# Kernel tuning notes

Measured on AMD Instinct MI355X. Metric: run time of the kernel, lower is better.

Reference implementation:

```python
import jax, jax.numpy as jnp
import numpy as np

D_MODEL = 1024


def setup_inputs() -> dict:
    key = jax.random.key(0)
    ks = jax.random.split(key, 7)
    x = jax.random.normal(ks[0], (4, 2048, D_MODEL), dtype=jnp.float32)
    scale = 1.0 / np.sqrt(D_MODEL)
    Wq = jax.random.normal(ks[1], (D_MODEL, D_MODEL), dtype=jnp.float32) * scale
    bq = jnp.zeros((D_MODEL,), dtype=jnp.float32)
    Wk = jax.random.normal(ks[2], (D_MODEL, D_MODEL), dtype=jnp.float32) * scale
    bk = jnp.zeros((D_MODEL,), dtype=jnp.float32)
    Wv = jax.random.normal(ks[3], (D_MODEL, D_MODEL), dtype=jnp.float32) * scale
    bv = jnp.zeros((D_MODEL,), dtype=jnp.float32)
    return {"x": x, "Wq": Wq, "bq": bq, "Wk": Wk, "bk": bk, "Wv": Wv, "bv": bv}


def reference(x, Wq, bq, Wk, bk, Wv, bv):
    # Linear layers: y = x @ W^T + b (torch nn.Linear convention)
    q = jnp.einsum("bsd,ed->bse", x, Wq) + bq
    k = jnp.einsum("bsd,ed->bse", x, Wk) + bk
    v = jnp.einsum("bsd,ed->bse", x, Wv) + bv
    d_k = q.shape[-1]
    inv_sqrt_dk = 1.0 / jnp.sqrt(jnp.float32(d_k))
    # [B, S, S] score matrix, softmax over keys, then AV
    score = jnp.einsum("bqd,bkd->bqk", q, k) * inv_sqrt_dk
    attn = jax.nn.softmax(score, axis=-1)
    out = jnp.einsum("bqk,bkd->bqd", attn, v)
    return out
```

## Files before the change

kernel.cpp:

```cpp
#include <hip/hip_runtime.h>
#include <hip/hip_bf16.h>


typedef __hip_bfloat16 bf16;
typedef __attribute__((ext_vector_type(8))) short bf16x8;
typedef __attribute__((ext_vector_type(4))) float f32x4;
typedef __attribute__((ext_vector_type(4))) short short4v;

__device__ __forceinline__ void gload16(const bf16* g, bf16* l) {
  __builtin_amdgcn_global_load_lds(
      (const __attribute__((address_space(1))) void*)g,
      (__attribute__((address_space(3))) void*)l, 16, 0, 0);
}

__global__ __launch_bounds__(256)
void cast_f32_to_bf16(const float* __restrict__ in, bf16* __restrict__ out) {
  long i = ((long)blockIdx.x * blockDim.x + threadIdx.x) * 4;
  float4 f = *(const float4*)(in + i);
  bf16 tmp[4];
  tmp[0] = __float2bfloat16(f.x);
  tmp[1] = __float2bfloat16(f.y);
  tmp[2] = __float2bfloat16(f.z);
  tmp[3] = __float2bfloat16(f.w);
  *(short4v*)(out + i) = *(short4v*)tmp;
}

__global__ __launch_bounds__(256)
void cast3_f32_to_bf16(const float* __restrict__ w0, const float* __restrict__ w1,
                       const float* __restrict__ w2, bf16* __restrict__ out) {
  const float* src = (blockIdx.y == 0) ? w0 : (blockIdx.y == 1) ? w1 : w2;
  long i = ((long)blockIdx.x * blockDim.x + threadIdx.x) * 4;
  float4 f = *(const float4*)(src + i);
  bf16 tmp[4];
  tmp[0] = __float2bfloat16(f.x);
  tmp[1] = __float2bfloat16(f.y);
  tmp[2] = __float2bfloat16(f.z);
  tmp[3] = __float2bfloat16(f.w);
  *(short4v*)(out + (long)blockIdx.y * 1024 * 1024 + i) = *(short4v*)tmp;
}

template<int OMODE>
__global__ __launch_bounds__(256, 3)
void gemm_bt(const bf16* __restrict__ A, const bf16* __restrict__ Bt,
             const float* __restrict__ b0, const float* __restrict__ b1,
             const float* __restrict__ b2, void* __restrict__ Cout,
             int K, int lda, int ldb, int ldc, float scale,
             long sA, long sB, long sC)
{
  __shared__ __align__(16) bf16 As[128 * 64];
  __shared__ __align__(16) bf16 Bs[128 * 64];
  const int tid = threadIdx.x;
  const int z = blockIdx.z;
  const bf16* Ab = A + (long)z * sA;
  const bf16* Bb = Bt + (long)z * sB;
  const long bm = (long)blockIdx.x * 128;
  const long bn = (long)blockIdx.y * 128;
  const int wid = tid >> 6;
  const int lane = tid & 63;
  const int wr = (wid >> 1) * 64;
  const int wc = (wid & 1) * 64;
  const int l15 = lane & 15;
  const int kg = lane >> 4;

  f32x4 acc[4][4];
#pragma unroll
  for (int m = 0; m < 4; ++m)
#pragma unroll
    for (int n = 0; n < 4; ++n)
      acc[m][n] = (f32x4){0.f, 0.f, 0.f, 0.f};

  for (int k0 = 0; k0 < K; k0 += 64) {
#pragma unroll
    for (int i = 0; i < 4; ++i) {
      const int c = (i << 8) + tid;
      const int r = c >> 3;
      const int j = (c & 7) ^ (r & 7);
      const int ldsch = (i << 8) + (wid << 6);
      gload16(Ab + (long)(bm + r) * lda + k0 + (j << 3), As + ldsch * 8);
      gload16(Bb + (long)(bn + r) * ldb + k0 + (j << 3), Bs + ldsch * 8);
    }
    __syncthreads();
#pragma unroll
    for (int kk = 0; kk < 2; ++kk) {
      bf16x8 af[4], bfv[4];
#pragma unroll
      for (int m = 0; m < 4; ++m) {
        const int row_l = wr + (m << 4) + l15;
        const int js = ((kk << 2) + kg) ^ (row_l & 7);
        af[m] = *(const bf16x8*)&As[(row_l << 6) + (js << 3)];
      }
#pragma unroll
      for (int n = 0; n < 4; ++n) {
        const int row_l = wc + (n << 4) + l15;
        const int js = ((kk << 2) + kg) ^ (row_l & 7);
        bfv[n] = *(const bf16x8*)&Bs[(row_l << 6) + (js << 3)];
      }
#pragma unroll
      for (int m = 0; m < 4; ++m)
#pragma unroll
        for (int n = 0; n < 4; ++n)
          acc[m][n] = __builtin_amdgcn_mfma_f32_16x16x32_bf16(
              af[m], bfv[n], acc[m][n], 0, 0, 0);
    }
    __syncthreads();
  }

#pragma unroll
  for (int m = 0; m < 4; ++m) {
    const long row0 = bm + wr + (m << 4) + (kg << 2);
#pragma unroll
    for (int n = 0; n < 4; ++n) {
      const long col = bn + wc + (n << 4) + l15;
      const float* bias = (z == 0) ? b0 : (z == 1) ? b1 : b2;
      const float bias_v = bias[col];
      if (z < 2) {
        bf16* C = (bf16*)Cout + (long)z * 8192 * 1024;
#pragma unroll
        for (int rr = 0; rr < 4; ++rr)
          C[(row0 + rr) * 1024 + col] =
              __float2bfloat16(acc[m][n][rr] + bias_v);
      } else {
        bf16* C = (bf16*)Cout + 2L * 8192 * 1024;
        const long bb = row0 >> 11;
        const long s0 = row0 & 2047;
        bf16 tmp[4];
#pragma unroll
        for (int rr = 0; rr < 4; ++rr)
          tmp[rr] = __float2bfloat16(acc[m][n][rr] + bias_v);
        *(short4v*)&C[(bb * 1024 + col) * 2048 + s0] = *(short4v*)tmp;
      }
    }
  }
}

template<int OMODE>
__global__ __launch_bounds__(512, 4)
void gemm8w(const bf16* __restrict__ A, const bf16* __restrict__ Bt,
            void* __restrict__ Cout, int K, int lda, int ldb, int ldc,
            float scale, long sA, long sB, long sC)
{
  __shared__ __align__(16) bf16 As[128 * 64 + 6144];
  __shared__ __align__(16) bf16 Bs[128 * 64 + 6144];
  const int tid = threadIdx.x;
  const int z = blockIdx.z;
  const bf16* Ab = A + (long)z * sA;
  const bf16* Bb = Bt + (long)z * sB;
  const long bm = (long)blockIdx.x * 128;
  const long bn = (long)blockIdx.y * 128;
  const int wid = tid >> 6;
  const int lane = tid & 63;
  const int wr = (wid >> 2) * 64;
  const int wc = (wid & 3) * 32;
  const int l15 = lane & 15;
  const int kg = lane >> 4;

  f32x4 acc[4][2];
#pragma unroll
  for (int m = 0; m < 4; ++m)
#pragma unroll
    for (int n = 0; n < 2; ++n)
      acc[m][n] = (f32x4){0.f, 0.f, 0.f, 0.f};

  for (int k0 = 0; k0 < K; k0 += 64) {
#pragma unroll
    for (int i = 0; i < 2; ++i) {
      const int c = (i << 9) + tid;
      const int r = c >> 3;
      const int j = (c & 7) ^ (r & 7);
      const int ldsch = (i << 9) + (wid << 6);
      gload16(Ab + (long)(bm + r) * lda + k0 + (j << 3), As + ldsch * 8);
      gload16(Bb + (long)(bn + r) * ldb + k0 + (j << 3), Bs + ldsch * 8);
    }
    __syncthreads();
#pragma unroll
    for (int kk = 0; kk < 2; ++kk) {
      bf16x8 af[4], bfv[2];
#pragma unroll
      for (int m = 0; m < 4; ++m) {
        const int row_l = wr + (m << 4) + l15;
        const int js = ((kk << 2) + kg) ^ (row_l & 7);
        af[m] = *(const bf16x8*)&As[(row_l << 6) + (js << 3)];
      }
#pragma unroll
      for (int n = 0; n < 2; ++n) {
        const int row_l = wc + (n << 4) + l15;
        const int js = ((kk << 2) + kg) ^ (row_l & 7);
        bfv[n] = *(const bf16x8*)&Bs[(row_l << 6) + (js << 3)];
      }
#pragma unroll
      for (int m = 0; m < 4; ++m)
#pragma unroll
        for (int n = 0; n < 2; ++n)
          acc[m][n] = __builtin_amdgcn_mfma_f32_16x16x32_bf16(
              af[m], bfv[n], acc[m][n], 0, 0, 0);
    }
    __syncthreads();
  }

#pragma unroll
  for (int m = 0; m < 4; ++m) {
    const long row0 = bm + wr + (m << 4) + (kg << 2);
#pragma unroll
    for (int n = 0; n < 2; ++n) {
      const long col = bn + wc + (n << 4) + l15;
      if constexpr (OMODE == 0) {
        float* C = (float*)Cout + (long)z * sC;
#pragma unroll
        for (int rr = 0; rr < 4; ++rr)
          C[(row0 + rr) * ldc + col] = acc[m][n][rr] * scale;
      } else {
        bf16* C = (bf16*)Cout + (long)z * sC;
#pragma unroll
        for (int rr = 0; rr < 4; ++rr)
          C[(row0 + rr) * ldc + col] = __float2bfloat16(acc[m][n][rr] * scale);
      }
    }
  }
}

__global__ __launch_bounds__(256)
void softmax_bf16(bf16* __restrict__ S) {
  bf16* row = S + (size_t)blockIdx.x * 2048;
  const int tid = threadIdx.x;
  __shared__ float redA[4], redB[4];
  bf16x8 in = *(const bf16x8*)(row + (tid << 3));
  float v[8];
  float mx = -1e30f;
#pragma unroll
  for (int i = 0; i < 8; ++i) {
    v[i] = __bfloat162float(((const bf16*)&in)[i]);
    mx = fmaxf(mx, v[i]);
  }
#pragma unroll
  for (int o = 32; o; o >>= 1) mx = fmaxf(mx, __shfl_xor(mx, o));
  if ((tid & 63) == 0) redA[tid >> 6] = mx;
  __syncthreads();
  mx = fmaxf(fmaxf(redA[0], redA[1]), fmaxf(redA[2], redA[3]));
  float sum = 0.f;
#pragma unroll
  for (int i = 0; i < 8; ++i) {
    v[i] = __expf(v[i] - mx);
    sum += v[i];
  }
#pragma unroll
  for (int o = 32; o; o >>= 1) sum += __shfl_xor(sum, o);
  if ((tid & 63) == 0) redB[tid >> 6] = sum;
  __syncthreads();
  sum = redB[0] + redB[1] + redB[2] + redB[3];
  const float inv = 1.f / sum;
  bf16 tmp[8];
#pragma unroll
  for (int i = 0; i < 8; ++i) tmp[i] = __float2bfloat16(v[i] * inv);
  *(bf16x8*)(row + (tid << 3)) = *(bf16x8*)tmp;
}

extern "C" void kernel_launch(void* const* d_in, const int* in_sizes, int n_in,
                              void* d_out, int out_size, void* d_ws, size_t ws_size,
                              hipStream_t stream) {
  const float* x  = (const float*)d_in[0];
  const float* Wq = (const float*)d_in[1];
  const float* bq = (const float*)d_in[2];
  const float* Wk = (const float*)d_in[3];
  const float* bk = (const float*)d_in[4];
  const float* Wv = (const float*)d_in[5];
  const float* bv = (const float*)d_in[6];
  float* out = (float*)d_out;

  const int B = 4, S = 2048, D = 1024;
  const int M = B * S;

  bf16* xb  = (bf16*)d_ws;
  bf16* wqb = xb + (size_t)M * D;
  bf16* qb  = wqb + 3 * (size_t)D * D;
  bf16* kb  = qb + (size_t)M * D;
  bf16* vtb = kb + (size_t)M * D;
  bf16* sc  = vtb + (size_t)M * D;

  size_t avail = ws_size - ((size_t)((char*)sc - (char*)d_ws));
  int nb = (int)(avail / ((size_t)S * S * 2));
  if (nb > B) nb = B;
  if (nb < 1) nb = 1;

  cast_f32_to_bf16<<<dim3(M * D / 1024), 256, 0, stream>>>(x, xb);
  cast3_f32_to_bf16<<<dim3(D * D / 1024, 3), 256, 0, stream>>>(Wq, Wk, Wv, wqb);

  gemm_bt<3><<<dim3(M / 128, D / 128, 3), 256, 0, stream>>>(
      xb, wqb, bq, bk, bv, qb, D, D, D, D, 1.f, 0, (long)D * D, 0);

  const float iscale = 1.0f / 32.0f;
  for (int g = 0; g < B; g += nb) {
    const int gn = (g + nb <= B) ? nb : (B - g);
    gemm8w<1><<<dim3(S / 128, S / 128, gn), 512, 0, stream>>>(
        qb + (size_t)g * S * D, kb + (size_t)g * S * D,
        sc, D, D, D, S, iscale, (long)S * D, (long)S * D, (long)S * S);
    softmax_bf16<<<dim3(gn * S), 256, 0, stream>>>(sc);
    gemm8w<0><<<dim3(S / 128, D / 128, gn), 512, 0, stream>>>(
        sc, vtb + (size_t)g * D * S,
        out + (size_t)g * S * D, S, S, S, D, 1.f,
        (long)S * S, (long)D * S, (long)S * D);
  }
}
```

Baseline: 172.3 us.

## Add 256x256 double-buffered phased GEMM kernel for QK^T score computation

Adds a new 8-wave kernel that computes the Q·K^T scores with 256x256 output tiles. It double-buffers LDS through direct global-to-LDS loads and splits each K step into four MFMA quadrants, interleaved with prefetches, explicit waitcnt, barriers and setprio. The aim is to hide global load latency behind MFMA work and to raise data reuse per tile. In exchange it uses 128KB of LDS and many accumulator registers, which limits occupancy to one block per CU, and it launches only 64 blocks per batch. The QKV and AV kernels get cleanup only: templates are removed and parameters simplified.

```diff
diff --git a/kernel.cpp b/kernel.cpp
--- a/kernel.cpp
+++ b/kernel.cpp
@@ -12,6 +12,13 @@
       (const __attribute__((address_space(1))) void*)g,
       (__attribute__((address_space(3))) void*)l, 16, 0, 0);
 }
+
+#define WAITV(N) asm volatile("s_waitcnt vmcnt(" #N ")" ::: "memory")
+#define LGKM0    asm volatile("s_waitcnt lgkmcnt(0)" ::: "memory")
+#define SCHED0   __builtin_amdgcn_sched_barrier(0)
+#define BAR      __builtin_amdgcn_s_barrier()
+#define PRIO1    __builtin_amdgcn_s_setprio(1)
+#define PRIO0    __builtin_amdgcn_s_setprio(0)
 
 __global__ __launch_bounds__(256)
 void cast_f32_to_bf16(const float* __restrict__ in, bf16* __restrict__ out) {
@@ -39,35 +46,29 @@
   *(short4v*)(out + (long)blockIdx.y * 1024 * 1024 + i) = *(short4v*)tmp;
 }
 
-template<int OMODE>
 __global__ __launch_bounds__(256, 3)
-void gemm_bt(const bf16* __restrict__ A, const bf16* __restrict__ Bt,
-             const float* __restrict__ b0, const float* __restrict__ b1,
-             const float* __restrict__ b2, void* __restrict__ Cout,
-             int K, int lda, int ldb, int ldc, float scale,
-             long sA, long sB, long sC)
+void gemm_qkv(const bf16* __restrict__ A, const bf16* __restrict__ Bt,
+              const float* __restrict__ b0, const float* __restrict__ b1,
+              const float* __restrict__ b2, void* __restrict__ Cout,
+              int K, int lda, int ldb, long sB)
 {
   __shared__ __align__(16) bf16 As[128 * 64];
   __shared__ __align__(16) bf16 Bs[128 * 64];
   const int tid = threadIdx.x;
   const int z = blockIdx.z;
-  const bf16* Ab = A + (long)z * sA;
+  const bf16* Ab = A;
   const bf16* Bb = Bt + (long)z * sB;
   const long bm = (long)blockIdx.x * 128;
   const long bn = (long)blockIdx.y * 128;
-  const int wid = tid >> 6;
-  const int lane = tid & 63;
-  const int wr = (wid >> 1) * 64;
-  const int wc = (wid & 1) * 64;
-  const int l15 = lane & 15;
-  const int kg = lane >> 4;
+  const int wid = tid >> 6, lane = tid & 63;
+  const int wr = (wid >> 1) * 64, wc = (wid & 1) * 64;
+  const int l15 = lane & 15, kg = lane >> 4;
 
   f32x4 acc[4][4];
 #pragma unroll
   for (int m = 0; m < 4; ++m)
 #pragma unroll
-    for (int n = 0; n < 4; ++n)
-      acc[m][n] = (f32x4){0.f, 0.f, 0.f, 0.f};
+    for (int n = 0; n < 4; ++n) acc[m][n] = (f32x4){0.f, 0.f, 0.f, 0.f};
 
   for (int k0 = 0; k0 < K; k0 += 64) {
 #pragma unroll
@@ -117,8 +118,7 @@
         bf16* C = (bf16*)Cout + (long)z * 8192 * 1024;
 #pragma unroll
         for (int rr = 0; rr < 4; ++rr)
-          C[(row0 + rr) * 1024 + col] =
-              __float2bfloat16(acc[m][n][rr] + bias_v);
+          C[(row0 + rr) * 1024 + col] = __float2bfloat16(acc[m][n][rr] + bias_v);
       } else {
         bf16* C = (bf16*)Cout + 2L * 8192 * 1024;
         const long bb = row0 >> 11;
@@ -134,6 +134,130 @@
 }
 
 template<int OMODE>
+__global__ __launch_bounds__(512)
+void gemm8ph(const bf16* __restrict__ A, const bf16* __restrict__ Bt,
+             void* __restrict__ Cout, int K, int lda, int ldb, int ldc,
+             float scale, long sA, long sB, long sC)
+{
+  __shared__ __align__(16) bf16 As[2][2][128 * 64];
+  __shared__ __align__(16) bf16 Bs[2][2][128 * 64];
+  const int tid = threadIdx.x;
+  const int wid = tid >> 6, lane = tid & 63;
+  const int l15 = lane & 15, kg = lane >> 4;
+  const int wr = wid >> 2;
+  const int wc = wid & 3;
+  const int bh = wc >> 1;
+  const int z = blockIdx.z;
+  const bf16* Ab = A + (long)z * sA;
+  const bf16* Bb = Bt + (long)z * sB;
+  const long bm = (long)blockIdx.x * 256;
+  const long bn = (long)blockIdx.y * 256;
+
+  const bf16* gAp[2][2];
+  const bf16* gBp[2][2];
+  int dOff[2];
+#pragma unroll
+  for (int l = 0; l < 2; ++l) {
+    const int c = (l << 9) + tid;
+    const int r = c >> 3;
+    const int j = (c & 7) ^ (r & 7);
+#pragma unroll
+    for (int h = 0; h < 2; ++h) {
+      gAp[h][l] = Ab + (long)(bm + h * 128 + r) * lda + (j << 3);
+      gBp[h][l] = Bb + (long)(bn + h * 128 + r) * ldb + (j << 3);
+    }
+    dOff[l] = (((l << 9) + (wid << 6)) << 3);
+  }
+#define STG_A(H, BUF, TT) do { const int _k = (TT) << 6;            \
+    gload16(gAp[H][0] + _k, &As[BUF][H][dOff[0]]);                  \
+    gload16(gAp[H][1] + _k, &As[BUF][H][dOff[1]]); } while (0)
+#define STG_B(H, BUF, TT) do { const int _k = (TT) << 6;            \
+    gload16(gBp[H][0] + _k, &Bs[BUF][H][dOff[0]]);                  \
+    gload16(gBp[H][1] + _k, &Bs[BUF][H][dOff[1]]); } while (0)
+
+  bf16x8 af[2][4], bv[2][2][2];
+  f32x4 acc[8][4];
+#pragma unroll
+  for (int m = 0; m < 8; ++m)
+#pragma unroll
+    for (int n = 0; n < 4; ++n) acc[m][n] = (f32x4){0.f, 0.f, 0.f, 0.f};
+
+#define READA(MH, BUF) do { _Pragma("unroll") for (int kk = 0; kk < 2; ++kk) \
+    _Pragma("unroll") for (int mi = 0; mi < 4; ++mi) {                       \
+      const int row = (MH) * 64 + mi * 16 + l15;                             \
+      const int js = ((kk << 2) + kg) ^ (row & 7);                           \
+      af[kk][mi] = *(const bf16x8*)&As[BUF][wr][(row << 6) + (js << 3)];     \
+    } } while (0)
+#define READB(NH, BUF) do { _Pragma("unroll") for (int kk = 0; kk < 2; ++kk) \
+    _Pragma("unroll") for (int ni = 0; ni < 2; ++ni) {                       \
+      const int row = (wc & 1) * 64 + ((NH) * 2 + ni) * 16 + l15;            \
+      const int js = ((kk << 2) + kg) ^ (row & 7);                           \
+      bv[NH][kk][ni] = *(const bf16x8*)&Bs[BUF][bh][(row << 6) + (js << 3)]; \
+    } } while (0)
+#define MFMAQ(MH, NH) do { _Pragma("unroll") for (int kk = 0; kk < 2; ++kk)  \
+    _Pragma("unroll") for (int mi = 0; mi < 4; ++mi)                         \
+    _Pragma("unroll") for (int ni = 0; ni < 2; ++ni)                         \
+      acc[(MH)*4+mi][(NH)*2+ni] = __builtin_amdgcn_mfma_f32_16x16x32_bf16(   \
+          af[kk][mi], bv[NH][kk][ni], acc[(MH)*4+mi][(NH)*2+ni], 0, 0, 0);   \
+  } while (0)
+
+  const int T = K >> 6;
+  STG_B(0, 0, 0); STG_B(1, 0, 0); STG_A(0, 0, 0); STG_A(1, 0, 0);
+  STG_B(0, 1, 1); STG_B(1, 1, 1);
+  WAITV(4); BAR;
+
+  for (int t = 0; t < T; t += 2) {
+    const bool pre = (t + 2) < T;
+    READA(0, 0); READB(0, 0);
+    STG_A(0, 1, t + 1);
+    BAR; LGKM0; SCHED0; PRIO1; MFMAQ(0, 0); PRIO0; BAR;
+    READB(1, 0);
+    STG_A(1, 1, t + 1);
+    BAR; LGKM0; SCHED0; PRIO1; MFMAQ(0, 1); PRIO0; BAR;
+    READA(1, 0);
+    if (pre) STG_B(0, 0, t + 2);
+    BAR; LGKM0; SCHED0; PRIO1; MFMAQ(1, 0); PRIO0; BAR;
+    if (pre) { STG_B(1, 0, t + 2); WAITV(4); } else { WAITV(0); }
+    BAR; PRIO1; MFMAQ(1, 1); PRIO0; BAR;
+    READA(0, 1); READB(0, 1);
+    if (pre) STG_A(0, 0, t + 2);
+    BAR; LGKM0; SCHED0; PRIO1; MFMAQ(0, 0); PRIO0; BAR;
+    READB(1, 1);
+    if (pre) STG_A(1, 0, t + 2);
+    BAR; LGKM0; SCHED0; PRIO1; MFMAQ(0, 1); PRIO0; BAR;
+    READA(1, 1);
+    if (pre) STG_B(0, 1, t + 3);
+    BAR; LGKM0; SCHED0; PRIO1; MFMAQ(1, 0); PRIO0; BAR;
+    if (pre) { STG_B(1, 1, t + 3); WAITV(4); }
+    BAR; PRIO1; MFMAQ(1, 1); PRIO0; BAR;
+  }
+#undef STG_A
+#undef STG_B
+#undef READA
+#undef READB
+#undef MFMAQ
+
+#pragma unroll
+  for (int m = 0; m < 8; ++m) {
+    const long row0 = bm + wr * 128 + m * 16 + (kg << 2);
+#pragma unroll
+    for (int n = 0; n < 4; ++n) {
+      const long col = bn + wc * 64 + n * 16 + l15;
+      if constexpr (OMODE == 0) {
+        float* C = (float*)Cout + (long)z * sC;
+#pragma unroll
+        for (int rr = 0; rr < 4; ++rr)
+          C[(row0 + rr) * ldc + col] = acc[m][n][rr] * scale;
+      } else {
+        bf16* C = (bf16*)Cout + (long)z * sC;
+#pragma unroll
+        for (int rr = 0; rr < 4; ++rr)
+          C[(row0 + rr) * ldc + col] = __float2bfloat16(acc[m][n][rr] * scale);
+      }
+    }
+  }
+}
+
 __global__ __launch_bounds__(512, 4)
 void gemm8w(const bf16* __restrict__ A, const bf16* __restrict__ Bt,
             void* __restrict__ Cout, int K, int lda, int ldb, int ldc,
@@ -147,19 +271,15 @@
   const bf16* Bb = Bt + (long)z * sB;
   const long bm = (long)blockIdx.x * 128;
   const long bn = (long)blockIdx.y * 128;
-  const int wid = tid >> 6;
-  const int lane = tid & 63;
-  const int wr = (wid >> 2) * 64;
-  const int wc = (wid & 3) * 32;
-  const int l15 = lane & 15;
-  const int kg = lane >> 4;
+  const int wid = tid >> 6, lane = tid & 63;
+  const int wr = (wid >> 2) * 64, wc = (wid & 3) * 32;
+  const int l15 = lane & 15, kg = lane >> 4;
 
   f32x4 acc[4][2];
 #pragma unroll
   for (int m = 0; m < 4; ++m)
 #pragma unroll
-    for (int n = 0; n < 2; ++n)
-      acc[m][n] = (f32x4){0.f, 0.f, 0.f, 0.f};
+    for (int n = 0; n < 2; ++n) acc[m][n] = (f32x4){0.f, 0.f, 0.f, 0.f};
 
   for (int k0 = 0; k0 < K; k0 += 64) {
 #pragma unroll
@@ -203,17 +323,10 @@
 #pragma unroll
     for (int n = 0; n < 2; ++n) {
       const long col = bn + wc + (n << 4) + l15;
-      if constexpr (OMODE == 0) {
-        float* C = (float*)Cout + (long)z * sC;
-#pragma unroll
-        for (int rr = 0; rr < 4; ++rr)
-          C[(row0 + rr) * ldc + col] = acc[m][n][rr] * scale;
-      } else {
-        bf16* C = (bf16*)Cout + (long)z * sC;
-#pragma unroll
-        for (int rr = 0; rr < 4; ++rr)
-          C[(row0 + rr) * ldc + col] = __float2bfloat16(acc[m][n][rr] * scale);
-      }
+      float* C = (float*)Cout + (long)z * sC;
+#pragma unroll
+      for (int rr = 0; rr < 4; ++rr)
+        C[(row0 + rr) * ldc + col] = acc[m][n][rr] * scale;
     }
   }
 }
@@ -284,17 +397,17 @@
   cast_f32_to_bf16<<<dim3(M * D / 1024), 256, 0, stream>>>(x, xb);
   cast3_f32_to_bf16<<<dim3(D * D / 1024, 3), 256, 0, stream>>>(Wq, Wk, Wv, wqb);
 
-  gemm_bt<3><<<dim3(M / 128, D / 128, 3), 256, 0, stream>>>(
-      xb, wqb, bq, bk, bv, qb, D, D, D, D, 1.f, 0, (long)D * D, 0);
+  gemm_qkv<<<dim3(M / 128, D / 128, 3), 256, 0, stream>>>(
+      xb, wqb, bq, bk, bv, qb, D, D, D, (long)D * D);
 
   const float iscale = 1.0f / 32.0f;
   for (int g = 0; g < B; g += nb) {
     const int gn = (g + nb <= B) ? nb : (B - g);
-    gemm8w<1><<<dim3(S / 128, S / 128, gn), 512, 0, stream>>>(
+    gemm8ph<1><<<dim3(S / 256, S / 256, gn), 512, 0, stream>>>(
         qb + (size_t)g * S * D, kb + (size_t)g * S * D,
         sc, D, D, D, S, iscale, (long)S * D, (long)S * D, (long)S * S);
     softmax_bf16<<<dim3(gn * S), 256, 0, stream>>>(sc);
-    gemm8w<0><<<dim3(S / 128, D / 128, gn), 512, 0, stream>>>(
+    gemm8w<<<dim3(S / 128, D / 128, gn), 512, 0, stream>>>(
         sc, vtb + (size_t)g * D * S,
         out + (size_t)g * S * D, S, S, S, D, 1.f,
         (long)S * S, (long)D * S, (long)S * D);
```

Result: no change. 169.8 us (-1.5%).
